# Kernel optimization log

Hardware: AMD Instinct MI355X
Metric: run time of the kernel (lower is better)

The kernel has to match this reference:

```python
import jax, jax.numpy as jnp
import numpy as np

IMG = 128          # image_size
TEX = 4            # texture_size (hard-coded in module)
WIDTH = float(np.tan(np.radians(30.0)))  # nr default viewing_angle=30
NEAR = 0.1
# images dict: values are [distance, azimuth, elevation]; eye = get_points_from_angles(dist, elev, azim)
VIEWS = [(2.83, 45.0, 0.0), (2.0, 0.0, 90.0), (3.46, 45.0, 45.0), (3.0, 0.0, 0.0)]  # (dist, elev, azim)


def _eye_from_angles(dist, elev_deg, azim_deg):
    e, a = np.radians(elev_deg), np.radians(azim_deg)
    return jnp.asarray([dist * np.cos(e) * np.sin(a), dist * np.sin(e), -dist * np.cos(e) * np.cos(a)], jnp.float32)


def _normalize(v):
    return v / jnp.linalg.norm(v)


def _trilinear(tex, c):
    # tex: [P, T, T, T, 3], c: [P, 3] continuous coords in [0, T-1]
    i0 = jnp.clip(jnp.floor(c).astype(jnp.int32), 0, TEX - 2)
    f = c - i0.astype(c.dtype)
    pi = jnp.arange(tex.shape[0])
    out = jnp.zeros((tex.shape[0], 3), tex.dtype)
    for dx in (0, 1):
        for dy in (0, 1):
            for dz in (0, 1):
                wgt = ((f[:, 0] if dx else 1.0 - f[:, 0])
                       * (f[:, 1] if dy else 1.0 - f[:, 1])
                       * (f[:, 2] if dz else 1.0 - f[:, 2]))
                out = out + wgt[:, None] * tex[pi, i0[:, 0] + dx, i0[:, 1] + dy, i0[:, 2] + dz]
    return out


def _render(verts, faces, tex, eye):
    # verts [V,3], faces [F,3] int, tex [F,T,T,T,3] -> image [1,3,IMG,IMG]
    # look_at transform (at=origin, up=+y)
    z_ax = _normalize(-eye)
    x_ax = _normalize(jnp.cross(jnp.asarray([0.0, 1.0, 0.0], jnp.float32), z_ax))
    y_ax = _normalize(jnp.cross(z_ax, x_ax))
    R = jnp.stack([x_ax, y_ax, z_ax])                       # [3,3]
    v = (verts - eye) @ R.T                                 # [V,3]
    # perspective projection
    z = v[:, 2]
    v = jnp.stack([v[:, 0] / (z * WIDTH), v[:, 1] / (z * WIDTH), z], -1)
    fv = v[faces]                                           # [F,3,3]

    # pixel grid in NDC [-1,1], row 0 = top
    s = (jnp.arange(IMG, dtype=jnp.float32) + 0.5) / IMG * 2.0 - 1.0
    px = jnp.broadcast_to(s[None, :], (IMG, IMG)).ravel()
    py = jnp.broadcast_to(-s[:, None], (IMG, IMG)).ravel()
    p = jnp.stack([px, py], -1)                             # [P,2]

    v0 = fv[:, 0, :2]
    e1 = fv[:, 1, :2] - v0
    e2 = fv[:, 2, :2] - v0
    det = e1[:, 0] * e2[:, 1] - e1[:, 1] * e2[:, 0]         # [F]
    ok = jnp.abs(det) > 1e-8
    inv_det = jnp.where(ok, 1.0 / jnp.where(ok, det, 1.0), 0.0)
    d = p[None, :, :] - v0[:, None, :]                      # [F,P,2]
    w1 = (e2[:, None, 1] * d[..., 0] - e2[:, None, 0] * d[..., 1]) * inv_det[:, None]
    w2 = (-e1[:, None, 1] * d[..., 0] + e1[:, None, 0] * d[..., 1]) * inv_det[:, None]
    w0 = 1.0 - w1 - w2
    fz = fv[:, :, 2]                                        # [F,3]
    depth = w0 * fz[:, 0:1] + w1 * fz[:, 1:2] + w2 * fz[:, 2:3]  # [F,P]
    visible = (w0 >= 0) & (w1 >= 0) & (w2 >= 0) & ok[:, None] & (depth > NEAR)
    depth_m = jnp.where(visible, depth, jnp.inf)
    fidx = jnp.argmin(depth_m, axis=0)                      # [P]
    P = fidx.shape[0]
    pi = jnp.arange(P)
    hit = jnp.isfinite(depth_m[fidx, pi])
    wsel = jnp.stack([w0[fidx, pi], w1[fidx, pi], w2[fidx, pi]], -1)  # [P,3]
    coords = jnp.clip(wsel, 0.0, 1.0) * (TEX - 1)
    color = _trilinear(tex[fidx], coords) * hit[:, None].astype(tex.dtype)  # [P,3]
    return color.reshape(IMG, IMG, 3).transpose(2, 0, 1)[None]  # [1,3,IMG,IMG]


def setup_inputs() -> dict:
    key = jax.random.key(0)
    k1, k2, k3, k4 = jax.random.split(key, 4)
    V, F = 1024, 1024
    vertices = jax.random.normal(k1, (1, V, 3), jnp.float32) * 0.5
    faces = jax.random.randint(k2, (1, F, 3), 0, V, jnp.int32)
    textures = jax.random.normal(k3, (1, F, TEX, TEX, TEX, 3), jnp.float32)
    image_refs = jax.random.uniform(k4, (4, 1, IMG, IMG), jnp.float32)
    return {"vertices": vertices, "faces": faces, "textures": textures, "image_refs": image_refs}


def reference(vertices, faces, textures, image_refs):
    tex = jnp.tanh(textures)[0]   # [F,T,T,T,3]
    verts = vertices[0]
    fcs = faces[0]
    loss = jnp.float32(0.0)
    for c, (dist, elev, azim) in enumerate(VIEWS):
        image = _render(verts, fcs, tex, _eye_from_angles(dist, elev, azim))  # [1,3,H,W]
        ref = image_refs[c][:, None]                                          # [1,1,H,W]
        loss = loss + jnp.sum((image - ref) ** 2)
    return loss
```

## Files before the change

kernel.cpp:

```cpp
#include <hip/hip_runtime.h>
#include <math.h>

#define IMG 128
#define NPIX (IMG * IMG)
#define NF 1024
#define NCHUNK 8
#define CHF 128
#define NEAR_Z 0.1f
#define DY 0.015625f

struct AllViews { float m[4][12]; };

__device__ __forceinline__ void project_face(
    const float* __restrict__ verts, const int* __restrict__ faces,
    const float* M, float W, int f, float proj[3][3])
{
#pragma unroll
    for (int k = 0; k < 3; ++k) {
        int vi = faces[f * 3 + k];
        float px = verts[vi * 3 + 0] - M[9];
        float py = verts[vi * 3 + 1] - M[10];
        float pz = verts[vi * 3 + 2] - M[11];
        float x = M[0] * px + M[1] * py + M[2] * pz;
        float y = M[3] * px + M[4] * py + M[5] * pz;
        float z = M[6] * px + M[7] * py + M[8] * pz;
        proj[k][0] = x / (z * W);
        proj[k][1] = y / (z * W);
        proj[k][2] = z;
    }
}

__device__ __forceinline__ void face_planes(const float proj[3][3],
    float& a1x, float& a1y, float& b1, float& a2x, float& a2y, float& b2,
    float& z0, float& g1, float& g2)
{
    float v0x = proj[0][0], v0y = proj[0][1];
    float e1x = proj[1][0] - v0x, e1y = proj[1][1] - v0y;
    float e2x = proj[2][0] - v0x, e2y = proj[2][1] - v0y;
    float det = e1x * e2y - e1y * e2x;
    bool ok = fabsf(det) > 1e-8f;
    float inv = ok ? 1.0f / det : 0.0f;
    a1x = e2y * inv; a1y = -e2x * inv;
    b1 = -(a1x * v0x + a1y * v0y);
    a2x = -e1y * inv; a2y = e1x * inv;
    b2 = -(a2x * v0x + a2y * v0y);
    z0 = ok ? proj[0][2] : 0.0f;
    g1 = proj[1][2] - proj[0][2];
    g2 = proj[2][2] - proj[0][2];
}

__device__ __forceinline__ float fast_tanh(float x)
{
    float xc = fminf(fmaxf(x, -10.0f), 10.0f);
    float e = __expf(2.0f * xc);
    return __fdividef(e - 1.0f, e + 1.0f);
}

__global__ __launch_bounds__(256) void raster(
    const float* __restrict__ verts, const int* __restrict__ faces,
    unsigned long long* __restrict__ keys, unsigned int* __restrict__ counter,
    AllViews vc, float W)
{
    __shared__ float4 P0[CHF];
    __shared__ float4 P1[CHF];
    __shared__ float  G2[CHF];
    __shared__ unsigned long long MASK[4][2];

    int bid = blockIdx.x;
    int view  = bid >> 7;
    int b     = bid & 127;
    int chunk = b & (NCHUNK - 1);
    int strip = b >> 3;
    int tid  = threadIdx.x;
    int wave = tid >> 6, lane = tid & 63;

    if (bid == 0 && tid == 0) *counter = 0;

    float ymin = INFINITY, ymax = -INFINITY;
    if (tid < CHF) {
        int f = chunk * CHF + tid;
        float proj[3][3];
        project_face(verts, faces, vc.m[view], W, f, proj);
        float a1x, a1y, b1, a2x, a2y, b2, z0, g1, g2;
        face_planes(proj, a1x, a1y, b1, a2x, a2y, b2, z0, g1, g2);
        P0[tid] = make_float4(a1x, a1y, b1, a2x);
        P1[tid] = make_float4(a2y, b2, z0, g1);
        G2[tid] = g2;
        if (z0 != 0.0f) {
            ymin = fminf(fminf(proj[0][1], proj[1][1]), proj[2][1]);
            ymax = fmaxf(fmaxf(proj[0][1], proj[1][1]), proj[2][1]);
        }
    }
    if (wave < 2) {
#pragma unroll
        for (int rp = 0; rp < 4; ++rp) {
            int r0 = strip * 8 + 2 * rp;
            float syhi = 1.0f - (r0 + 0.5f) * DY;
            float sylo = syhi - DY;
            bool inter = (ymin <= syhi) && (ymax >= sylo);
            unsigned long long m = __ballot(inter);
            if (lane == 0) MASK[rp][wave] = m;
        }
    }
    __syncthreads();

    int r0 = strip * 8 + 2 * wave;
    float sy0 = 1.0f - (r0 + 0.5f) * DY;
    float sx0 = (lane + 0.5f) * DY - 1.0f;

    float bst[4] = {INFINITY, INFINITY, INFINITY, INFINITY};
    int   bfi[4] = {0, 0, 0, 0};

#pragma unroll
    for (int half = 0; half < 2; ++half) {
        unsigned long long m = MASK[wave][half];
        int fbase = half * 64;
        while (m) {
            int f = fbase + (int)__builtin_ctzll(m);
            m &= m - 1;
            float4 q0 = P0[f];
            float4 q1 = P1[f];
            float g2  = G2[f];
            float w1_00 = fmaf(q0.x, sx0, fmaf(q0.y, sy0, q0.z));
            float w2_00 = fmaf(q0.w, sx0, fmaf(q1.x, sy0, q1.y));
            float w1_01 = w1_00 + q0.x;
            float w2_01 = w2_00 + q0.w;
            float w1_10 = fmaf(q0.y, -DY, w1_00);
            float w2_10 = fmaf(q1.x, -DY, w2_00);
            float w1_11 = w1_10 + q0.x;
            float w2_11 = w2_10 + q0.w;
            float w1q[4] = {w1_00, w1_01, w1_10, w1_11};
            float w2q[4] = {w2_00, w2_01, w2_10, w2_11};
#pragma unroll
            for (int q = 0; q < 4; ++q) {
                float w1 = w1q[q], w2 = w2q[q];
                float dep = fmaf(w2, g2, fmaf(w1, q1.w, q1.z));
                bool vis = (fminf(w1, w2) >= 0.0f) && (w1 + w2 <= 1.0f) &&
                           (dep > NEAR_Z);
                bool take = vis && (dep < bst[q]);
                bst[q] = take ? dep : bst[q];
                bfi[q] = take ? f : bfi[q];
            }
        }
    }

    size_t base = ((size_t)(view * NCHUNK + chunk) << 14);
    int p00 = r0 * IMG + lane;
    int fo = chunk * CHF;
#pragma unroll
    for (int q = 0; q < 4; ++q) {
        unsigned long long key =
            ((unsigned long long)__float_as_uint(bst[q]) << 32) |
            (unsigned int)(fo + bfi[q]);
        keys[base + p00 + (q & 1) * 64 + (q >> 1) * IMG] = key;
    }
}

__global__ __launch_bounds__(256) void shade_loss(
    const float* __restrict__ verts, const int* __restrict__ faces,
    const unsigned long long* __restrict__ keys,
    const float* __restrict__ tex,
    const float* __restrict__ refs,
    float* __restrict__ partial, unsigned int* __restrict__ counter,
    float* __restrict__ out, AllViews vc, float W)
{
    __shared__ float wsum[4];
    __shared__ bool last;
    int tid = threadIdx.x;
    int t = blockIdx.x * 256 + tid;
    int view = t >> 14, p = t & (NPIX - 1);
    int row = p >> 7, col = p & 127;
    float sx = (col + 0.5f) * DY - 1.0f;
    float sy = 1.0f - (row + 0.5f) * DY;

    const unsigned long long* kb = keys + ((size_t)(view * NCHUNK) << 14) + p;
    unsigned long long key = ~0ULL;
#pragma unroll
    for (int c = 0; c < NCHUNK; ++c) {
        unsigned long long k = kb[(size_t)c << 14];
        key = (k < key) ? k : key;
    }

    bool hit = (unsigned int)(key >> 32) < 0x7f800000u;
    float ref = refs[t];
    float lossv;
    if (hit) {
        int f = (int)(key & 0xffffffffu);
        float proj[3][3];
        project_face(verts, faces, vc.m[view], W, f, proj);
        float a1x, a1y, b1, a2x, a2y, b2, z0, g1, g2;
        face_planes(proj, a1x, a1y, b1, a2x, a2y, b2, z0, g1, g2);
        float w1 = fmaf(a1x, sx, fmaf(a1y, sy, b1));
        float w2 = fmaf(a2x, sx, fmaf(a2y, sy, b2));
        float w0 = 1.0f - w1 - w2;
        float cx = fminf(fmaxf(w0, 0.0f), 1.0f) * 3.0f;
        float cy = fminf(fmaxf(w1, 0.0f), 1.0f) * 3.0f;
        float cz = fminf(fmaxf(w2, 0.0f), 1.0f) * 3.0f;
        int ix = min(max((int)floorf(cx), 0), 2);
        int iy = min(max((int)floorf(cy), 0), 2);
        int iz = min(max((int)floorf(cz), 0), 2);
        float fx = cx - (float)ix, fy = cy - (float)iy, fz = cz - (float)iz;

        const float* T = tex + (size_t)f * 192;
        float c0 = 0.0f, c1 = 0.0f, c2 = 0.0f;
#pragma unroll
        for (int dxi = 0; dxi < 2; ++dxi)
#pragma unroll
            for (int dyi = 0; dyi < 2; ++dyi)
#pragma unroll
                for (int dzi = 0; dzi < 2; ++dzi) {
                    float w = (dxi ? fx : 1.0f - fx) *
                              (dyi ? fy : 1.0f - fy) *
                              (dzi ? fz : 1.0f - fz);
                    int base = (((ix + dxi) * 4 + (iy + dyi)) * 4 + (iz + dzi)) * 3;
                    c0 += w * fast_tanh(T[base + 0]);
                    c1 += w * fast_tanh(T[base + 1]);
                    c2 += w * fast_tanh(T[base + 2]);
                }
        float d0 = c0 - ref, d1 = c1 - ref, d2 = c2 - ref;
        lossv = d0 * d0 + d1 * d1 + d2 * d2;
    } else {
        lossv = 3.0f * ref * ref;
    }

    for (int off = 32; off; off >>= 1) lossv += __shfl_down(lossv, off);
    if ((tid & 63) == 0) wsum[tid >> 6] = lossv;
    __syncthreads();
    if (tid == 0) {
        partial[blockIdx.x] = wsum[0] + wsum[1] + wsum[2] + wsum[3];
        __threadfence();
        unsigned int old = atomicAdd(counter, 1);
        last = (old == (unsigned int)(gridDim.x - 1));
    }
    __syncthreads();
    if (last) {
        __threadfence();
        float v = partial[tid];
        for (int off = 32; off; off >>= 1) v += __shfl_down(v, off);
        if ((tid & 63) == 0) wsum[tid >> 6] = v;
        __syncthreads();
        if (tid == 0) out[0] = wsum[0] + wsum[1] + wsum[2] + wsum[3];
    }
}

static void make_view(double dist, double elev, double azim, float* M)
{
    double e = elev * M_PI / 180.0, a = azim * M_PI / 180.0;
    float ex = (float)(dist * cos(e) * sin(a));
    float ey = (float)(dist * sin(e));
    float ez = (float)(-dist * cos(e) * cos(a));
    float zx = -ex, zy = -ey, zz = -ez;
    float n = sqrtf(zx * zx + zy * zy + zz * zz);
    zx /= n; zy /= n; zz /= n;
    float xx = zz, xy = 0.0f, xz = -zx;
    n = sqrtf(xx * xx + xy * xy + xz * xz);
    xx /= n; xy /= n; xz /= n;
    float yx = zy * xz - zz * xy;
    float yy = zz * xx - zx * xz;
    float yz = zx * xy - zy * xx;
    n = sqrtf(yx * yx + yy * yy + yz * yz);
    yx /= n; yy /= n; yz /= n;
    M[0] = xx; M[1] = xy; M[2] = xz;
    M[3] = yx; M[4] = yy; M[5] = yz;
    M[6] = zx; M[7] = zy; M[8] = zz;
    M[9] = ex; M[10] = ey; M[11] = ez;
}

extern "C" void kernel_launch(void* const* d_in, const int* in_sizes, int n_in,
                              void* d_out, int out_size, void* d_ws, size_t ws_size,
                              hipStream_t stream)
{
    const float* verts = (const float*)d_in[0];
    const int*   faces = (const int*)d_in[1];
    const float* tex   = (const float*)d_in[2];
    const float* refs  = (const float*)d_in[3];
    float* out = (float*)d_out;

    char* ws = (char*)d_ws;
    unsigned long long* keys = (unsigned long long*)ws;
    ws += (size_t)4 * NCHUNK * NPIX * sizeof(unsigned long long);
    float* partial = (float*)ws;
    ws += 256 * sizeof(float);
    unsigned int* counter = (unsigned int*)ws;

    AllViews vc;
    const double V[4][3] = {{2.83, 45.0, 0.0}, {2.0, 0.0, 90.0},
                            {3.46, 45.0, 45.0}, {3.0, 0.0, 0.0}};
    for (int i = 0; i < 4; ++i) make_view(V[i][0], V[i][1], V[i][2], vc.m[i]);
    float W = (float)tan(M_PI / 6.0);

    raster<<<512, 256, 0, stream>>>(verts, faces, keys, counter, vc, W);
    shade_loss<<<256, 256, 0, stream>>>(verts, faces, keys, tex, refs,
                                        partial, counter, out, vc, W);
}
```

Before: 44.39 us.

## Precompute per-face projection planes once in a separate kernel

Adds a precompute kernel that projects each face for all four views once and stores plane coefficients and y-bounds in a workspace buffer. The raster kernel now copies these from global memory into LDS instead of reprojecting faces in each of the 16 strip blocks per chunk. The shade kernel reads the stored coefficients instead of recomputing projection per hit pixel. This trades redundant ALU and gather work for an extra kernel launch and more global memory traffic.

```diff
diff --git a/kernel.cpp b/kernel.cpp
--- a/kernel.cpp
+++ b/kernel.cpp
@@ -11,10 +11,26 @@
 
 struct AllViews { float m[4][12]; };
 
-__device__ __forceinline__ void project_face(
-    const float* __restrict__ verts, const int* __restrict__ faces,
-    const float* M, float W, int f, float proj[3][3])
-{
+__device__ __forceinline__ float fast_tanh(float x)
+{
+    float xc = fminf(fmaxf(x, -10.0f), 10.0f);
+    float e = __expf(2.0f * xc);
+    return __fdividef(e - 1.0f, e + 1.0f);
+}
+
+__global__ void precompute(const float* __restrict__ verts,
+                           const int* __restrict__ faces,
+                           float4* __restrict__ fd,
+                           unsigned int* __restrict__ counter,
+                           AllViews vc, float W)
+{
+    int t = blockIdx.x * blockDim.x + threadIdx.x;
+    if (t == 0) *counter = 0;
+    if (t >= 4 * NF) return;
+    int view = t >> 10, f = t & (NF - 1);
+    const float* M = vc.m[view];
+
+    float proj[3][3];
 #pragma unroll
     for (int k = 0; k < 3; ++k) {
         int vi = faces[f * 3 + k];
@@ -28,42 +44,35 @@
         proj[k][1] = y / (z * W);
         proj[k][2] = z;
     }
-}
-
-__device__ __forceinline__ void face_planes(const float proj[3][3],
-    float& a1x, float& a1y, float& b1, float& a2x, float& a2y, float& b2,
-    float& z0, float& g1, float& g2)
-{
     float v0x = proj[0][0], v0y = proj[0][1];
     float e1x = proj[1][0] - v0x, e1y = proj[1][1] - v0y;
     float e2x = proj[2][0] - v0x, e2y = proj[2][1] - v0y;
     float det = e1x * e2y - e1y * e2x;
     bool ok = fabsf(det) > 1e-8f;
     float inv = ok ? 1.0f / det : 0.0f;
-    a1x = e2y * inv; a1y = -e2x * inv;
-    b1 = -(a1x * v0x + a1y * v0y);
-    a2x = -e1y * inv; a2y = e1x * inv;
-    b2 = -(a2x * v0x + a2y * v0y);
-    z0 = ok ? proj[0][2] : 0.0f;
-    g1 = proj[1][2] - proj[0][2];
-    g2 = proj[2][2] - proj[0][2];
-}
-
-__device__ __forceinline__ float fast_tanh(float x)
-{
-    float xc = fminf(fmaxf(x, -10.0f), 10.0f);
-    float e = __expf(2.0f * xc);
-    return __fdividef(e - 1.0f, e + 1.0f);
+    float a1x = e2y * inv, a1y = -e2x * inv;
+    float b1 = -(a1x * v0x + a1y * v0y);
+    float a2x = -e1y * inv, a2y = e1x * inv;
+    float b2 = -(a2x * v0x + a2y * v0y);
+    float z0 = ok ? proj[0][2] : 0.0f;
+    float g1 = proj[1][2] - proj[0][2];
+    float g2 = proj[2][2] - proj[0][2];
+    float ymin = INFINITY, ymax = -INFINITY;
+    if (ok) {
+        ymin = fminf(fminf(proj[0][1], proj[1][1]), proj[2][1]);
+        ymax = fmaxf(fmaxf(proj[0][1], proj[1][1]), proj[2][1]);
+    }
+    float4* o = fd + (size_t)t * 3;
+    o[0] = make_float4(a1x, a1y, b1, a2x);
+    o[1] = make_float4(a2y, b2, z0, g1);
+    o[2] = make_float4(g2, ymin, ymax, 0.0f);
 }
 
 __global__ __launch_bounds__(256) void raster(
-    const float* __restrict__ verts, const int* __restrict__ faces,
-    unsigned long long* __restrict__ keys, unsigned int* __restrict__ counter,
-    AllViews vc, float W)
-{
-    __shared__ float4 P0[CHF];
-    __shared__ float4 P1[CHF];
-    __shared__ float  G2[CHF];
+    const float4* __restrict__ fd,
+    unsigned long long* __restrict__ keys)
+{
+    __shared__ float4 lds4[CHF * 3];
     __shared__ unsigned long long MASK[4][2];
 
     int bid = blockIdx.x;
@@ -74,31 +83,18 @@
     int tid  = threadIdx.x;
     int wave = tid >> 6, lane = tid & 63;
 
-    if (bid == 0 && tid == 0) *counter = 0;
-
-    float ymin = INFINITY, ymax = -INFINITY;
-    if (tid < CHF) {
-        int f = chunk * CHF + tid;
-        float proj[3][3];
-        project_face(verts, faces, vc.m[view], W, f, proj);
-        float a1x, a1y, b1, a2x, a2y, b2, z0, g1, g2;
-        face_planes(proj, a1x, a1y, b1, a2x, a2y, b2, z0, g1, g2);
-        P0[tid] = make_float4(a1x, a1y, b1, a2x);
-        P1[tid] = make_float4(a2y, b2, z0, g1);
-        G2[tid] = g2;
-        if (z0 != 0.0f) {
-            ymin = fminf(fminf(proj[0][1], proj[1][1]), proj[2][1]);
-            ymax = fmaxf(fmaxf(proj[0][1], proj[1][1]), proj[2][1]);
-        }
-    }
+    const float4* src = fd + (size_t)(view * NF + chunk * CHF) * 3;
+    for (int i = tid; i < CHF * 3; i += 256) lds4[i] = src[i];
+    __syncthreads();
+
     if (wave < 2) {
+        float4 bb = lds4[(wave * 64 + lane) * 3 + 2];
 #pragma unroll
         for (int rp = 0; rp < 4; ++rp) {
             int r0 = strip * 8 + 2 * rp;
             float syhi = 1.0f - (r0 + 0.5f) * DY;
             float sylo = syhi - DY;
-            bool inter = (ymin <= syhi) && (ymax >= sylo);
-            unsigned long long m = __ballot(inter);
+            unsigned long long m = __ballot((bb.y <= syhi) && (bb.z >= sylo));
             if (lane == 0) MASK[rp][wave] = m;
         }
     }
@@ -110,6 +106,7 @@
 
     float bst[4] = {INFINITY, INFINITY, INFINITY, INFINITY};
     int   bfi[4] = {0, 0, 0, 0};
+    const float* ldsf = (const float*)lds4;
 
 #pragma unroll
     for (int half = 0; half < 2; ++half) {
@@ -118,9 +115,9 @@
         while (m) {
             int f = fbase + (int)__builtin_ctzll(m);
             m &= m - 1;
-            float4 q0 = P0[f];
-            float4 q1 = P1[f];
-            float g2  = G2[f];
+            float4 q0 = lds4[f * 3 + 0];
+            float4 q1 = lds4[f * 3 + 1];
+            float g2  = ldsf[f * 12 + 8];
             float w1_00 = fmaf(q0.x, sx0, fmaf(q0.y, sy0, q0.z));
             float w2_00 = fmaf(q0.w, sx0, fmaf(q1.x, sy0, q1.y));
             float w1_01 = w1_00 + q0.x;
@@ -157,12 +154,12 @@
 }
 
 __global__ __launch_bounds__(256) void shade_loss(
-    const float* __restrict__ verts, const int* __restrict__ faces,
+    const float4* __restrict__ fd,
     const unsigned long long* __restrict__ keys,
     const float* __restrict__ tex,
     const float* __restrict__ refs,
     float* __restrict__ partial, unsigned int* __restrict__ counter,
-    float* __restrict__ out, AllViews vc, float W)
+    float* __restrict__ out)
 {
     __shared__ float wsum[4];
     __shared__ bool last;
@@ -186,12 +183,11 @@
     float lossv;
     if (hit) {
         int f = (int)(key & 0xffffffffu);
-        float proj[3][3];
-        project_face(verts, faces, vc.m[view], W, f, proj);
-        float a1x, a1y, b1, a2x, a2y, b2, z0, g1, g2;
-        face_planes(proj, a1x, a1y, b1, a2x, a2y, b2, z0, g1, g2);
-        float w1 = fmaf(a1x, sx, fmaf(a1y, sy, b1));
-        float w2 = fmaf(a2x, sx, fmaf(a2y, sy, b2));
+        const float4* Q = fd + (size_t)(view * NF + f) * 3;
+        float4 q0 = Q[0];
+        float4 q1 = Q[1];
+        float w1 = fmaf(q0.x, sx, fmaf(q0.y, sy, q0.z));
+        float w2 = fmaf(q0.w, sx, fmaf(q1.x, sy, q1.y));
         float w0 = 1.0f - w1 - w2;
         float cx = fminf(fmaxf(w0, 0.0f), 1.0f) * 3.0f;
         float cy = fminf(fmaxf(w1, 0.0f), 1.0f) * 3.0f;
@@ -277,6 +273,8 @@
     float* out = (float*)d_out;
 
     char* ws = (char*)d_ws;
+    float4* fd = (float4*)ws;
+    ws += (size_t)4 * NF * 3 * sizeof(float4);
     unsigned long long* keys = (unsigned long long*)ws;
     ws += (size_t)4 * NCHUNK * NPIX * sizeof(unsigned long long);
     float* partial = (float*)ws;
@@ -289,7 +287,8 @@
     for (int i = 0; i < 4; ++i) make_view(V[i][0], V[i][1], V[i][2], vc.m[i]);
     float W = (float)tan(M_PI / 6.0);
 
-    raster<<<512, 256, 0, stream>>>(verts, faces, keys, counter, vc, W);
-    shade_loss<<<256, 256, 0, stream>>>(verts, faces, keys, tex, refs,
-                                        partial, counter, out, vc, W);
-}
+    precompute<<<16, 256, 0, stream>>>(verts, faces, fd, counter, vc, W);
+    raster<<<512, 256, 0, stream>>>(fd, keys);
+    shade_loss<<<256, 256, 0, stream>>>(fd, keys, tex, refs,
+                                        partial, counter, out);
+}
```

Result: slower. 48.77 us (+9.9%).
